# Optimization experiments

Hardware: AMD Instinct MI355X
Metric: run time of the kernel (lower is better)

The kernel has to match this reference:

```python
import jax, jax.numpy as jnp
import numpy as np

HEADS = 4
DIM_HEAD = 32


def setup_inputs() -> dict:
    key = jax.random.key(0)
    k1, k2, k3, k4, k5 = jax.random.split(key, 5)
    dim = 128
    hidden = HEADS * DIM_HEAD  # 128
    h = w = 384
    x = jax.random.normal(k1, (1, dim, h, w), dtype=jnp.float32)
    # 1x1 conv weights (eqx Conv2d layout: [out_c, in_c, 1, 1]) + biases
    w_qkv = jax.random.normal(k2, (3 * hidden, dim, 1, 1), dtype=jnp.float32) * (1.0 / np.sqrt(dim))
    b_qkv = jax.random.normal(k3, (3 * hidden,), dtype=jnp.float32) * 0.01
    w_out = jax.random.normal(k4, (dim, hidden, 1, 1), dtype=jnp.float32) * (1.0 / np.sqrt(hidden))
    b_out = jax.random.normal(k5, (dim,), dtype=jnp.float32) * 0.01
    return {"x": x, "w_qkv": w_qkv, "b_qkv": b_qkv, "w_out": w_out, "b_out": b_out}


def reference(x, w_qkv, b_qkv, w_out, b_out):
    b, c, h, w = x.shape  # b == 1 (module squeezes batch)
    xs = x[0]  # (c, h, w)
    # 1x1 conv == channel matmul
    qkv = jnp.einsum('oc,chw->ohw', w_qkv[:, :, 0, 0], xs) + b_qkv[:, None, None]
    # rearrange '(qkv heads c) h w -> qkv heads c (h w)'
    qkv = qkv.reshape(3, HEADS, DIM_HEAD, h * w)
    q, k, v = qkv[0], qkv[1], qkv[2]  # each (heads, d, n)
    k = jax.nn.softmax(k, axis=-1)
    # context: (heads, d, e) -- small per-head outer product accumulated over n
    context = jnp.einsum('hdn,hen->hde', k, v)
    out = jnp.einsum('hde,hdn->hen', context, q)  # (heads, e, n)
    out = out.reshape(HEADS * DIM_HEAD, h, w)
    y = jnp.einsum('oc,chw->ohw', w_out[:, :, 0, 0], out) + b_out[:, None, None]
    return y  # (dim, h, w) -- module returns squeezed output
```

## Files before the change

### kernel.cpp

```cpp
#include <hip/hip_runtime.h>
#include <hip/hip_bf16.h>
#include <stdint.h>


#define NPOS 147456
#define NTILES 2304
#define NB1 512

typedef __attribute__((ext_vector_type(8))) short short8;
typedef __attribute__((ext_vector_type(4))) float floatx4;

__device__ __forceinline__ uint16_t f2bf(float f) {
    uint32_t u = __float_as_uint(f);
    return (uint16_t)((u + 0x7fffu + ((u >> 16) & 1u)) >> 16);
}
__device__ __forceinline__ uint32_t pack2(float a, float b) {
#if __has_builtin(__builtin_amdgcn_cvt_pk_bf16_f32)
    auto r = __builtin_amdgcn_cvt_pk_bf16_f32(a, b);
    uint32_t u; __builtin_memcpy(&u, &r, sizeof(u));
    return u;
#else
    return (uint32_t)f2bf(a) | ((uint32_t)f2bf(b) << 16);
#endif
}

#define XS_STRIDE 68
#define PS_STRIDE 36
#define WST_STRIDE 132

__device__ __forceinline__ void k1_load(const float* __restrict__ xb, float* pf) {
    #pragma unroll
    for (int i = 0; i < 32; ++i) pf[i] = xb[(size_t)i * NPOS];
}
__device__ __forceinline__ void k1_store(uint32_t* Xsbuf, const float* pf, int lane, int c0) {
    #pragma unroll
    for (int i = 0; i < 8; ++i) {
        uint2 w;
        w.x = pack2(pf[i * 4 + 0], pf[i * 4 + 1]);
        w.y = pack2(pf[i * 4 + 2], pf[i * 4 + 3]);
        *(uint2*)&Xsbuf[lane * XS_STRIDE + (c0 + i * 4) / 2] = w;
    }
}
__device__ __forceinline__ void k1_tile(
    const uint32_t* __restrict__ Xsbuf, uint32_t* __restrict__ Psw,
    const short8 (&wfr)[4][4], const float (&biasv)[4],
    floatx4 (&acc2)[4], float (&sacc)[2], int m, int quad)
{
    #pragma unroll
    for (int nt = 0; nt < 4; ++nt) {
        short8 afr[4];
        #pragma unroll
        for (int ks = 0; ks < 4; ++ks)
            afr[ks] = *(const short8*)&Xsbuf[(nt * 16 + m) * XS_STRIDE + ks * 16 + quad * 4];
        floatx4 pa[4];
        #pragma unroll
        for (int kt = 0; kt < 4; ++kt) pa[kt] = (floatx4){0.f, 0.f, 0.f, 0.f};
        #pragma unroll
        for (int ks = 0; ks < 4; ++ks)
            #pragma unroll
            for (int kt = 0; kt < 4; ++kt)
                pa[kt] = __builtin_amdgcn_mfma_f32_16x16x32_bf16(afr[ks], wfr[kt][ks], pa[kt], 0, 0, 0);
        #pragma unroll
        for (int kt = 0; kt < 4; ++kt) {
            float v0 = pa[kt][0] + biasv[kt];
            float v1 = pa[kt][1] + biasv[kt];
            float v2 = pa[kt][2] + biasv[kt];
            float v3 = pa[kt][3] + biasv[kt];
            if (kt < 2) {
                v0 = __expf(v0); v1 = __expf(v1);
                v2 = __expf(v2); v3 = __expf(v3);
                sacc[kt] += (v0 + v1) + (v2 + v3);
            }
            uint2 w;
            w.x = pack2(v0, v1);
            w.y = pack2(v2, v3);
            *(uint2*)&Psw[(kt * 16 + m) * PS_STRIDE + nt * 8 + quad * 2] = w;
        }
    }
    #pragma unroll
    for (int ks = 0; ks < 2; ++ks) {
        short8 ea[2], vb[2];
        #pragma unroll
        for (int dt = 0; dt < 2; ++dt)
            ea[dt] = *(const short8*)&Psw[(dt * 16 + m) * PS_STRIDE + ks * 16 + quad * 4];
        #pragma unroll
        for (int et = 0; et < 2; ++et)
            vb[et] = *(const short8*)&Psw[(32 + et * 16 + m) * PS_STRIDE + ks * 16 + quad * 4];
        #pragma unroll
        for (int dt = 0; dt < 2; ++dt)
            #pragma unroll
            for (int et = 0; et < 2; ++et)
                acc2[dt * 2 + et] = __builtin_amdgcn_mfma_f32_16x16x32_bf16(ea[dt], vb[et], acc2[dt * 2 + et], 0, 0, 0);
    }
}

__global__ __launch_bounds__(256, 2) void k1_ctx(
    const float* __restrict__ x, const float* __restrict__ w_qkv,
    const float* __restrict__ b_qkv, float* __restrict__ ctxP, int nb1)
{
    __shared__ uint32_t smem[2 * 64 * XS_STRIDE + 256 * PS_STRIDE];
    uint32_t* const Xs0 = smem;
    uint32_t* const Xs1 = smem + 64 * XS_STRIDE;
    uint32_t* const Ps  = smem + 2 * 64 * XS_STRIDE;

    const int t = threadIdx.x;
    const int lane = t & 63;
    const int wavu = __builtin_amdgcn_readfirstlane(t >> 6);
    const int m = lane & 15, quad = lane >> 4;
    const int c0 = wavu * 32;
    uint32_t* const Psw = &Ps[wavu * 64 * PS_STRIDE];

    const int T0 = NTILES / nb1, R = NTILES % nb1;
    const int b = blockIdx.x;
    const int cnt_tiles = T0 + (b < R ? 1 : 0);
    const int s0 = (b < R) ? b * (T0 + 1) : R * (T0 + 1) + (b - R) * T0;

    const float* xw = x + (size_t)c0 * NPOS + lane;
    float pfA[32], pfB[32];

    k1_load(xw + (size_t)s0 * 64, pfA);

    short8 wfr[4][4];
    float biasv[4];
    float* const Wst = (float*)smem + wavu * (32 * WST_STRIDE);
    #pragma unroll
    for (int pass = 0; pass < 2; ++pass) {
        const int rbase = (pass == 0 ? 128 : 256) + wavu * 32;
        const float* g = w_qkv + (size_t)rbase * 128;
        #pragma unroll
        for (int i = 0; i < 64; ++i) {
            const int idx = i * 64 + lane;
            Wst[(idx >> 7) * WST_STRIDE + (idx & 127)] = g[idx];
        }
        __syncthreads();
        #pragma unroll
        for (int kt = 0; kt < 2; ++kt) {
            const int lr = kt * 16 + m;
            #pragma unroll
            for (int ks = 0; ks < 4; ++ks) {
                const float* p = &Wst[lr * WST_STRIDE + ks * 32 + quad * 8];
                float4 a = *(const float4*)p;
                float4 c = *(const float4*)(p + 4);
                short8 w;
                w[0] = (short)f2bf(a.x); w[1] = (short)f2bf(a.y);
                w[2] = (short)f2bf(a.z); w[3] = (short)f2bf(a.w);
                w[4] = (short)f2bf(c.x); w[5] = (short)f2bf(c.y);
                w[6] = (short)f2bf(c.z); w[7] = (short)f2bf(c.w);
                wfr[pass * 2 + kt][ks] = w;
            }
            biasv[pass * 2 + kt] = b_qkv[rbase + kt * 16 + m];
        }
        __syncthreads();
    }

    floatx4 acc2[4];
    #pragma unroll
    for (int i = 0; i < 4; ++i) acc2[i] = (floatx4){0.f, 0.f, 0.f, 0.f};
    float sacc[2] = {0.f, 0.f};

    if (cnt_tiles > 1) k1_load(xw + (size_t)(s0 + 1) * 64, pfB);
    k1_store(Xs0, pfA, lane, c0);
    __syncthreads();

    for (int i = 0; i < cnt_tiles; i += 2) {
        if (i + 2 < cnt_tiles) k1_load(xw + (size_t)(s0 + i + 2) * 64, pfA);
        k1_tile(Xs0, Psw, wfr, biasv, acc2, sacc, m, quad);
        if (i + 1 < cnt_tiles) k1_store(Xs1, pfB, lane, c0);
        __syncthreads();
        if (i + 1 < cnt_tiles) {
            if (i + 3 < cnt_tiles) k1_load(xw + (size_t)(s0 + i + 3) * 64, pfB);
            k1_tile(Xs1, Psw, wfr, biasv, acc2, sacc, m, quad);
            if (i + 2 < cnt_tiles) k1_store(Xs0, pfA, lane, c0);
            __syncthreads();
        }
    }

    float* __restrict__ dst = ctxP + (size_t)(b & 7) * 4224;
    #pragma unroll
    for (int dt = 0; dt < 2; ++dt)
        #pragma unroll
        for (int et = 0; et < 2; ++et)
            #pragma unroll
            for (int r = 0; r < 4; ++r) {
                const int d = dt * 16 + quad * 4 + r, e = et * 16 + m;
                atomicAdd(&dst[wavu * 1024 + d * 32 + e], acc2[dt * 2 + et][r]);
            }
    #pragma unroll
    for (int kt = 0; kt < 2; ++kt) {
        float s = sacc[kt];
        s += __shfl_down(s, 32, 64);
        s += __shfl_down(s, 16, 64);
        if (lane < 16) atomicAdd(&dst[4096 + wavu * 32 + kt * 16 + lane], s);
    }
}

__global__ __launch_bounds__(256) void k2bc(
    const float* __restrict__ ctxP, const float* __restrict__ w_out,
    const float* __restrict__ w_qkv, const float* __restrict__ b_qkv,
    const float* __restrict__ b_out, uint32_t* __restrict__ Bmb, float* __restrict__ cvec)
{
    __shared__ float ctx33[128 * 33];
    __shared__ float Ss[128];
    __shared__ float Arow[128];
    __shared__ float row[128];
    __shared__ float red[128];
    const int o = blockIdx.x, t = threadIdx.x;
    for (int j = t; j < 4224; j += 256) {
        float s = 0.f;
        #pragma unroll
        for (int p = 0; p < 8; ++p) s += ctxP[p * 4224 + j];
        if (j < 4096) ctx33[(j >> 5) * 33 + (j & 31)] = s;
        else          Ss[j - 4096] = s;
    }
    __syncthreads();
    if (t < 128) {
        const int h = t >> 5;
        float s = 0.f;
        #pragma unroll
        for (int e = 0; e < 32; ++e)
            s = fmaf(w_out[o * 128 + h * 32 + e], ctx33[t * 33 + e], s);
        Arow[t] = s / Ss[t];
    }
    __syncthreads();
    if (t < 128) {
        float s = 0.f;
        #pragma unroll 16
        for (int hd = 0; hd < 128; ++hd)
            s = fmaf(Arow[hd], w_qkv[hd * 128 + t], s);
        row[t] = s;
        red[t] = Arow[t] * b_qkv[t];
    }
    __syncthreads();
    if (t < 64) Bmb[o * 64 + t] = pack2(row[2 * t], row[2 * t + 1]);
    if (t == 0) {
        float cs = b_out[o];
        #pragma unroll 8
        for (int i = 0; i < 128; ++i) cs += red[i];
        cvec[o] = cs;
    }
}

__global__ __launch_bounds__(256) void k3(
    const float* __restrict__ x, const uint32_t* __restrict__ Bmb,
    const float* __restrict__ cvec, float* __restrict__ y)
{
    __shared__ uint32_t Xs[64 * XS_STRIDE];
    const int t = threadIdx.x, lane = t & 63;
    const int wavu = __builtin_amdgcn_readfirstlane(t >> 6);
    const int m = lane & 15, quad = lane >> 4;
    const int n0 = blockIdx.x * 64;
    const int c0 = wavu * 32;

    float pf[32];
    k1_load(x + (size_t)c0 * NPOS + n0 + lane, pf);

    short8 bfr[2][4];
    float cv[2];
    #pragma unroll
    for (int ot = 0; ot < 2; ++ot) {
        const int o = (wavu * 2 + ot) * 16 + m;
        cv[ot] = cvec[o];
        #pragma unroll
        for (int ks = 0; ks < 4; ++ks)
            bfr[ot][ks] = *(const short8*)&Bmb[o * 64 + ks * 16 + quad * 4];
    }
    k1_store(Xs, pf, lane, c0);
    __syncthreads();

    floatx4 acc[2][4];
    #pragma unroll
    for (int ot = 0; ot < 2; ++ot)
        #pragma unroll
        for (int nt = 0; nt < 4; ++nt) acc[ot][nt] = (floatx4){0.f, 0.f, 0.f, 0.f};
    #pragma unroll
    for (int nt = 0; nt < 4; ++nt) {
        short8 afr[4];
        #pragma unroll
        for (int ks = 0; ks < 4; ++ks)
            afr[ks] = *(const short8*)&Xs[(nt * 16 + m) * XS_STRIDE + ks * 16 + quad * 4];
        #pragma unroll
        for (int ks = 0; ks < 4; ++ks)
            #pragma unroll
            for (int ot = 0; ot < 2; ++ot)
                acc[ot][nt] = __builtin_amdgcn_mfma_f32_16x16x32_bf16(afr[ks], bfr[ot][ks], acc[ot][nt], 0, 0, 0);
    }
    #pragma unroll
    for (int ot = 0; ot < 2; ++ot) {
        const int o = (wavu * 2 + ot) * 16 + m;
        #pragma unroll
        for (int nt = 0; nt < 4; ++nt) {
            floatx4 v = acc[ot][nt];
            v.x += cv[ot]; v.y += cv[ot]; v.z += cv[ot]; v.w += cv[ot];
            *(floatx4*)(y + (size_t)o * NPOS + n0 + nt * 16 + quad * 4) = v;
        }
    }
}

extern "C" void kernel_launch(void* const* d_in, const int* in_sizes, int n_in,
                              void* d_out, int out_size, void* d_ws, size_t ws_size,
                              hipStream_t stream)
{
    const float* x     = (const float*)d_in[0];
    const float* w_qkv = (const float*)d_in[1];
    const float* b_qkv = (const float*)d_in[2];
    const float* w_out = (const float*)d_in[3];
    const float* b_out = (const float*)d_in[4];
    float* y = (float*)d_out;

    char* wsb = (char*)d_ws;
    float* ctxP    = (float*)wsb;
    uint32_t* Bmb  = (uint32_t*)(wsb + (size_t)8 * 4224 * 4);
    float* cvec    = (float*)(wsb + (size_t)8 * 4224 * 4 + (size_t)8192 * 4);

    hipMemsetAsync(ctxP, 0, (size_t)8 * 4224 * sizeof(float), stream);
    hipLaunchKernelGGL(k1_ctx, dim3(NB1), dim3(256), 0, stream, x, w_qkv, b_qkv, ctxP, NB1);
    hipLaunchKernelGGL(k2bc, dim3(128), dim3(256), 0, stream, ctxP, w_out, w_qkv, b_qkv, b_out, Bmb, cvec);
    hipLaunchKernelGGL(k3, dim3(NTILES), dim3(256), 0, stream, x, Bmb, cvec, y);
}
```

Measured before the change: 183.5 us.

## Fuse three kernels into one cooperative persistent kernel with grid syncs

Merges the context-reduction, weight-folding and output-projection kernels into one cooperative kernel that separates the phases with grid-wide barriers. Intermediate values are exchanged through relaxed agent-scope atomics. The output phase becomes persistent, with each block looping over several tiles and prefetching the next one. This is meant to remove kernel launch gaps and tail effects, at the cost of grid-sync overhead and idle blocks during the small middle phase. If the cooperative launch is not possible, it falls back to three separate kernels.

After: 261.9 us. +42.7%, slower.

```diff
diff --git a/kernel.cpp b/kernel.cpp
--- a/kernel.cpp
+++ b/kernel.cpp
@@ -1,7 +1,10 @@
 #include <hip/hip_runtime.h>
+#include <hip/hip_cooperative_groups.h>
 #include <hip/hip_bf16.h>
 #include <stdint.h>
 
+
+namespace cg = cooperative_groups;
 
 #define NPOS 147456
 #define NTILES 2304
@@ -22,6 +25,22 @@
 #else
     return (uint32_t)f2bf(a) | ((uint32_t)f2bf(b) << 16);
 #endif
+}
+
+__device__ __forceinline__ float aloadf(const float* p) {
+    return __hip_atomic_load(p, __ATOMIC_RELAXED, __HIP_MEMORY_SCOPE_AGENT);
+}
+__device__ __forceinline__ void astoref(float* p, float v) {
+    __hip_atomic_store(p, v, __ATOMIC_RELAXED, __HIP_MEMORY_SCOPE_AGENT);
+}
+__device__ __forceinline__ void astoreu(uint32_t* p, uint32_t v) {
+    __hip_atomic_store(p, v, __ATOMIC_RELAXED, __HIP_MEMORY_SCOPE_AGENT);
+}
+__device__ __forceinline__ short8 aload_s8(const uint32_t* p) {
+    union { uint64_t u[2]; short8 s; } c;
+    c.u[0] = __hip_atomic_load((const uint64_t*)p,       __ATOMIC_RELAXED, __HIP_MEMORY_SCOPE_AGENT);
+    c.u[1] = __hip_atomic_load((const uint64_t*)(p + 2), __ATOMIC_RELAXED, __HIP_MEMORY_SCOPE_AGENT);
+    return c.s;
 }
 
 #define XS_STRIDE 68
@@ -94,24 +113,17 @@
     }
 }
 
-__global__ __launch_bounds__(256, 2) void k1_ctx(
-    const float* __restrict__ x, const float* __restrict__ w_qkv,
-    const float* __restrict__ b_qkv, float* __restrict__ ctxP, int nb1)
-{
-    __shared__ uint32_t smem[2 * 64 * XS_STRIDE + 256 * PS_STRIDE];
+__device__ __forceinline__ void phase1(
+    uint32_t* smem, const float* __restrict__ x, const float* __restrict__ w_qkv,
+    const float* __restrict__ b_qkv, float* __restrict__ ctxP, int nb1,
+    int b, int t, int lane, int wavu, int m, int quad, int c0)
+{
     uint32_t* const Xs0 = smem;
     uint32_t* const Xs1 = smem + 64 * XS_STRIDE;
     uint32_t* const Ps  = smem + 2 * 64 * XS_STRIDE;
-
-    const int t = threadIdx.x;
-    const int lane = t & 63;
-    const int wavu = __builtin_amdgcn_readfirstlane(t >> 6);
-    const int m = lane & 15, quad = lane >> 4;
-    const int c0 = wavu * 32;
     uint32_t* const Psw = &Ps[wavu * 64 * PS_STRIDE];
 
     const int T0 = NTILES / nb1, R = NTILES % nb1;
-    const int b = blockIdx.x;
     const int cnt_tiles = T0 + (b < R ? 1 : 0);
     const int s0 = (b < R) ? b * (T0 + 1) : R * (T0 + 1) + (b - R) * T0;
 
@@ -194,21 +206,21 @@
     }
 }
 
-__global__ __launch_bounds__(256) void k2bc(
-    const float* __restrict__ ctxP, const float* __restrict__ w_out,
+__device__ __forceinline__ void phase3(
+    uint32_t* smem, const float* __restrict__ ctxP, const float* __restrict__ w_out,
     const float* __restrict__ w_qkv, const float* __restrict__ b_qkv,
-    const float* __restrict__ b_out, uint32_t* __restrict__ Bmb, float* __restrict__ cvec)
-{
-    __shared__ float ctx33[128 * 33];
-    __shared__ float Ss[128];
-    __shared__ float Arow[128];
-    __shared__ float row[128];
-    __shared__ float red[128];
-    const int o = blockIdx.x, t = threadIdx.x;
+    const float* __restrict__ b_out, uint32_t* __restrict__ Bmb,
+    float* __restrict__ cvec, int o, int t)
+{
+    float* const ctx33 = (float*)smem;
+    float* const Ss    = ctx33 + 128 * 33;
+    float* const Arow  = Ss + 128;
+    float* const rowS  = Arow + 128;
+    float* const red   = rowS + 128;
     for (int j = t; j < 4224; j += 256) {
         float s = 0.f;
         #pragma unroll
-        for (int p = 0; p < 8; ++p) s += ctxP[p * 4224 + j];
+        for (int p = 0; p < 8; ++p) s += aloadf(&ctxP[p * 4224 + j]);
         if (j < 4096) ctx33[(j >> 5) * 33 + (j & 31)] = s;
         else          Ss[j - 4096] = s;
     }
@@ -227,73 +239,133 @@
         #pragma unroll 16
         for (int hd = 0; hd < 128; ++hd)
             s = fmaf(Arow[hd], w_qkv[hd * 128 + t], s);
-        row[t] = s;
+        rowS[t] = s;
         red[t] = Arow[t] * b_qkv[t];
     }
     __syncthreads();
-    if (t < 64) Bmb[o * 64 + t] = pack2(row[2 * t], row[2 * t + 1]);
+    if (t < 64) astoreu(&Bmb[o * 64 + t], pack2(rowS[2 * t], rowS[2 * t + 1]));
     if (t == 0) {
         float cs = b_out[o];
         #pragma unroll 8
         for (int i = 0; i < 128; ++i) cs += red[i];
-        cvec[o] = cs;
-    }
-}
-
-__global__ __launch_bounds__(256) void k3(
-    const float* __restrict__ x, const uint32_t* __restrict__ Bmb,
-    const float* __restrict__ cvec, float* __restrict__ y)
-{
-    __shared__ uint32_t Xs[64 * XS_STRIDE];
+        astoref(&cvec[o], cs);
+    }
+}
+
+__device__ __forceinline__ void phase4(
+    uint32_t* smem, const float* __restrict__ x, const uint32_t* __restrict__ Bmb,
+    const float* __restrict__ cvec, float* __restrict__ y, int nb1,
+    int b, int lane, int wavu, int m, int quad, int c0)
+{
+    uint32_t* const Xs3 = smem;
+    const int T3 = NTILES / nb1, R3 = NTILES % nb1;
+    const int cnt3 = T3 + (b < R3 ? 1 : 0);
+    const int s03 = (b < R3) ? b * (T3 + 1) : R3 * (T3 + 1) + (b - R3) * T3;
+
+    short8 bfr[2][4];
+    float cv[2];
+    #pragma unroll
+    for (int ot = 0; ot < 2; ++ot) {
+        const int o = (wavu * 2 + ot) * 16 + m;
+        cv[ot] = aloadf(&cvec[o]);
+        #pragma unroll
+        for (int ks = 0; ks < 4; ++ks)
+            bfr[ot][ks] = aload_s8(&Bmb[o * 64 + ks * 16 + quad * 4]);
+    }
+
+    float pf[32];
+    k1_load(x + (size_t)c0 * NPOS + (size_t)s03 * 64 + lane, pf);
+
+    for (int s = 0; s < cnt3; ++s) {
+        if (s) __syncthreads();
+        k1_store(Xs3, pf, lane, c0);
+        __syncthreads();
+        if (s + 1 < cnt3)
+            k1_load(x + (size_t)c0 * NPOS + (size_t)(s03 + s + 1) * 64 + lane, pf);
+
+        const int n0 = (s03 + s) * 64;
+        floatx4 acc[2][4];
+        #pragma unroll
+        for (int ot = 0; ot < 2; ++ot)
+            #pragma unroll
+            for (int nt = 0; nt < 4; ++nt) acc[ot][nt] = (floatx4){0.f, 0.f, 0.f, 0.f};
+        #pragma unroll
+        for (int nt = 0; nt < 4; ++nt) {
+            short8 afr[4];
+            #pragma unroll
+            for (int ks = 0; ks < 4; ++ks)
+                afr[ks] = *(const short8*)&Xs3[(nt * 16 + m) * XS_STRIDE + ks * 16 + quad * 4];
+            #pragma unroll
+            for (int ks = 0; ks < 4; ++ks)
+                #pragma unroll
+                for (int ot = 0; ot < 2; ++ot)
+                    acc[ot][nt] = __builtin_amdgcn_mfma_f32_16x16x32_bf16(afr[ks], bfr[ot][ks], acc[ot][nt], 0, 0, 0);
+        }
+        #pragma unroll
+        for (int ot = 0; ot < 2; ++ot) {
+            const int o = (wavu * 2 + ot) * 16 + m;
+            #pragma unroll
+            for (int nt = 0; nt < 4; ++nt) {
+                floatx4 v = acc[ot][nt];
+                v.x += cv[ot]; v.y += cv[ot]; v.z += cv[ot]; v.w += cv[ot];
+                *(floatx4*)(y + (size_t)o * NPOS + n0 + nt * 16 + quad * 4) = v;
+            }
+        }
+    }
+}
+
+__global__ __launch_bounds__(256, 2) void mono(
+    const float* __restrict__ x, const float* __restrict__ w_qkv,
+    const float* __restrict__ b_qkv, const float* __restrict__ w_out,
+    const float* __restrict__ b_out, float* __restrict__ ctxP,
+    uint32_t* __restrict__ Bmb, float* __restrict__ cvec,
+    float* __restrict__ y, int nb1)
+{
+    __shared__ uint32_t smem[2 * 64 * XS_STRIDE + 256 * PS_STRIDE];
+    const int t = threadIdx.x;
+    const int lane = t & 63;
+    const int wavu = __builtin_amdgcn_readfirstlane(t >> 6);
+    const int m = lane & 15, quad = lane >> 4;
+    const int c0 = wavu * 32;
+    const int b = blockIdx.x;
+
+    phase1(smem, x, w_qkv, b_qkv, ctxP, nb1, b, t, lane, wavu, m, quad, c0);
+    cg::this_grid().sync();
+    if (b < 128) phase3(smem, ctxP, w_out, w_qkv, b_qkv, b_out, Bmb, cvec, b, t);
+    cg::this_grid().sync();
+    phase4(smem, x, Bmb, cvec, y, nb1, b, lane, wavu, m, quad, c0);
+}
+
+__global__ __launch_bounds__(256, 2) void k1s(
+    const float* __restrict__ x, const float* __restrict__ w_qkv,
+    const float* __restrict__ b_qkv, float* __restrict__ ctxP, int nb1)
+{
+    __shared__ uint32_t smem[2 * 64 * XS_STRIDE + 256 * PS_STRIDE];
     const int t = threadIdx.x, lane = t & 63;
     const int wavu = __builtin_amdgcn_readfirstlane(t >> 6);
-    const int m = lane & 15, quad = lane >> 4;
-    const int n0 = blockIdx.x * 64;
-    const int c0 = wavu * 32;
-
-    float pf[32];
-    k1_load(x + (size_t)c0 * NPOS + n0 + lane, pf);
-
-    short8 bfr[2][4];
-    float cv[2];
-    #pragma unroll
-    for (int ot = 0; ot < 2; ++ot) {
-        const int o = (wavu * 2 + ot) * 16 + m;
-        cv[ot] = cvec[o];
-        #pragma unroll
-        for (int ks = 0; ks < 4; ++ks)
-            bfr[ot][ks] = *(const short8*)&Bmb[o * 64 + ks * 16 + quad * 4];
-    }
-    k1_store(Xs, pf, lane, c0);
-    __syncthreads();
-
-    floatx4 acc[2][4];
-    #pragma unroll
-    for (int ot = 0; ot < 2; ++ot)
-        #pragma unroll
-        for (int nt = 0; nt < 4; ++nt) acc[ot][nt] = (floatx4){0.f, 0.f, 0.f, 0.f};
-    #pragma unroll
-    for (int nt = 0; nt < 4; ++nt) {
-        short8 afr[4];
-        #pragma unroll
-        for (int ks = 0; ks < 4; ++ks)
-            afr[ks] = *(const short8*)&Xs[(nt * 16 + m) * XS_STRIDE + ks * 16 + quad * 4];
-        #pragma unroll
-        for (int ks = 0; ks < 4; ++ks)
-            #pragma unroll
-            for (int ot = 0; ot < 2; ++ot)
-                acc[ot][nt] = __builtin_amdgcn_mfma_f32_16x16x32_bf16(afr[ks], bfr[ot][ks], acc[ot][nt], 0, 0, 0);
-    }
-    #pragma unroll
-    for (int ot = 0; ot < 2; ++ot) {
-        const int o = (wavu * 2 + ot) * 16 + m;
-        #pragma unroll
-        for (int nt = 0; nt < 4; ++nt) {
-            floatx4 v = acc[ot][nt];
-            v.x += cv[ot]; v.y += cv[ot]; v.z += cv[ot]; v.w += cv[ot];
-            *(floatx4*)(y + (size_t)o * NPOS + n0 + nt * 16 + quad * 4) = v;
-        }
-    }
+    phase1(smem, x, w_qkv, b_qkv, ctxP, nb1, blockIdx.x, t, lane, wavu,
+           lane & 15, lane >> 4, wavu * 32);
+}
+
+__global__ __launch_bounds__(256) void k2s(
+    const float* __restrict__ ctxP, const float* __restrict__ w_out,
+    const float* __restrict__ w_qkv, const float* __restrict__ b_qkv,
+    const float* __restrict__ b_out, uint32_t* __restrict__ Bmb,
+    float* __restrict__ cvec)
+{
+    __shared__ uint32_t smem[4736];
+    phase3(smem, ctxP, w_out, w_qkv, b_qkv, b_out, Bmb, cvec, blockIdx.x, threadIdx.x);
+}
+
+__global__ __launch_bounds__(256) void k3s(
+    const float* __restrict__ x, const uint32_t* __restrict__ Bmb,
+    const float* __restrict__ cvec, float* __restrict__ y, int nb1)
+{
+    __shared__ uint32_t smem[64 * XS_STRIDE];
+    const int t = threadIdx.x, lane = t & 63;
+    const int wavu = __builtin_amdgcn_readfirstlane(t >> 6);
+    phase4(smem, x, Bmb, cvec, y, nb1, blockIdx.x, lane, wavu,
+           lane & 15, lane >> 4, wavu * 32);
 }
 
 extern "C" void kernel_launch(void* const* d_in, const int* in_sizes, int n_in,
@@ -313,7 +385,27 @@
     float* cvec    = (float*)(wsb + (size_t)8 * 4224 * 4 + (size_t)8192 * 4);
 
     hipMemsetAsync(ctxP, 0, (size_t)8 * 4224 * sizeof(float), stream);
-    hipLaunchKernelGGL(k1_ctx, dim3(NB1), dim3(256), 0, stream, x, w_qkv, b_qkv, ctxP, NB1);
-    hipLaunchKernelGGL(k2bc, dim3(128), dim3(256), 0, stream, ctxP, w_out, w_qkv, b_qkv, b_out, Bmb, cvec);
-    hipLaunchKernelGGL(k3, dim3(NTILES), dim3(256), 0, stream, x, Bmb, cvec, y);
-}
+
+    static int coopBlocks = -1;
+    if (coopBlocks < 0) {
+        int nb = 0;
+        hipError_t e = hipOccupancyMaxActiveBlocksPerMultiprocessor(&nb, mono, 256, 0);
+        coopBlocks = (e == hipSuccess) ? nb * 256 : 0;
+    }
+
+    int grid = coopBlocks > NB1 ? NB1 : coopBlocks;
+    if (grid >= 256) {
+        int nb1c = grid;
+        void* args[] = { (void*)&x, (void*)&w_qkv, (void*)&b_qkv, (void*)&w_out,
+                         (void*)&b_out, (void*)&ctxP, (void*)&Bmb, (void*)&cvec,
+                         (void*)&y, (void*)&nb1c };
+        hipError_t e = hipLaunchCooperativeKernel((void*)mono, dim3(grid), dim3(256),
+                                                  args, 0, stream);
+        if (e == hipSuccess) return;
+        (void)hipGetLastError();
+    }
+
+    hipLaunchKernelGGL(k1s, dim3(NB1), dim3(256), 0, stream, x, w_qkv, b_qkv, ctxP, NB1);
+    hipLaunchKernelGGL(k2s, dim3(128), dim3(256), 0, stream, ctxP, w_out, w_qkv, b_qkv, b_out, Bmb, cvec);
+    hipLaunchKernelGGL(k3s, dim3(NB1), dim3(256), 0, stream, x, Bmb, cvec, y, NB1);
+}
```

## Fuse context reduction and output-matrix build into k1 via last-block counter

Applied to the files above, without the earlier changes.

Removes the separate k2bc launch by having the last k1 block, detected via an atomic completion counter, sum the partial contexts and compute the folded output weight matrix and bias vector. This saves one kernel launch and its gap. In exchange, that tail work runs serially on a single 256-thread block, processing output rows in four chunks of 32, where k2bc previously spread it over 128 blocks.

After: 310.7 us. +69.3%, slower.

```diff
diff --git a/kernel.cpp b/kernel.cpp
--- a/kernel.cpp
+++ b/kernel.cpp
@@ -22,6 +22,9 @@
 #else
     return (uint32_t)f2bf(a) | ((uint32_t)f2bf(b) << 16);
 #endif
+}
+__device__ __forceinline__ float aloadf(const float* p) {
+    return __hip_atomic_load(p, __ATOMIC_RELAXED, __HIP_MEMORY_SCOPE_AGENT);
 }
 
 #define XS_STRIDE 68
@@ -94,149 +97,172 @@
     }
 }
 
-__global__ __launch_bounds__(256, 2) void k1_ctx(
+__global__ __launch_bounds__(256, 2) void k1f(
     const float* __restrict__ x, const float* __restrict__ w_qkv,
-    const float* __restrict__ b_qkv, float* __restrict__ ctxP, int nb1)
+    const float* __restrict__ b_qkv, const float* __restrict__ w_out,
+    const float* __restrict__ b_out, float* __restrict__ ctxP,
+    int* __restrict__ cnt, uint32_t* __restrict__ Bmb,
+    float* __restrict__ cvec, int nb1)
 {
     __shared__ uint32_t smem[2 * 64 * XS_STRIDE + 256 * PS_STRIDE];
-    uint32_t* const Xs0 = smem;
-    uint32_t* const Xs1 = smem + 64 * XS_STRIDE;
-    uint32_t* const Ps  = smem + 2 * 64 * XS_STRIDE;
+    __shared__ int lastFlag;
 
     const int t = threadIdx.x;
     const int lane = t & 63;
     const int wavu = __builtin_amdgcn_readfirstlane(t >> 6);
     const int m = lane & 15, quad = lane >> 4;
     const int c0 = wavu * 32;
-    uint32_t* const Psw = &Ps[wavu * 64 * PS_STRIDE];
-
-    const int T0 = NTILES / nb1, R = NTILES % nb1;
     const int b = blockIdx.x;
-    const int cnt_tiles = T0 + (b < R ? 1 : 0);
-    const int s0 = (b < R) ? b * (T0 + 1) : R * (T0 + 1) + (b - R) * T0;
-
-    const float* xw = x + (size_t)c0 * NPOS + lane;
-    float pfA[32], pfB[32];
-
-    k1_load(xw + (size_t)s0 * 64, pfA);
-
-    short8 wfr[4][4];
-    float biasv[4];
-    float* const Wst = (float*)smem + wavu * (32 * WST_STRIDE);
-    #pragma unroll
-    for (int pass = 0; pass < 2; ++pass) {
-        const int rbase = (pass == 0 ? 128 : 256) + wavu * 32;
-        const float* g = w_qkv + (size_t)rbase * 128;
-        #pragma unroll
-        for (int i = 0; i < 64; ++i) {
-            const int idx = i * 64 + lane;
-            Wst[(idx >> 7) * WST_STRIDE + (idx & 127)] = g[idx];
-        }
+
+    {
+        uint32_t* const Xs0 = smem;
+        uint32_t* const Xs1 = smem + 64 * XS_STRIDE;
+        uint32_t* const Ps  = smem + 2 * 64 * XS_STRIDE;
+        uint32_t* const Psw = &Ps[wavu * 64 * PS_STRIDE];
+
+        const int T0 = NTILES / nb1, R = NTILES % nb1;
+        const int cnt_tiles = T0 + (b < R ? 1 : 0);
+        const int s0 = (b < R) ? b * (T0 + 1) : R * (T0 + 1) + (b - R) * T0;
+
+        const float* xw = x + (size_t)c0 * NPOS + lane;
+        float pfA[32], pfB[32];
+
+        k1_load(xw + (size_t)s0 * 64, pfA);
+
+        short8 wfr[4][4];
+        float biasv[4];
+        float* const Wst = (float*)smem + wavu * (32 * WST_STRIDE);
+        #pragma unroll
+        for (int pass = 0; pass < 2; ++pass) {
+            const int rbase = (pass == 0 ? 128 : 256) + wavu * 32;
+            const float* g = w_qkv + (size_t)rbase * 128;
+            #pragma unroll
+            for (int i = 0; i < 64; ++i) {
+                const int idx = i * 64 + lane;
+                Wst[(idx >> 7) * WST_STRIDE + (idx & 127)] = g[idx];
+            }
+            __syncthreads();
+            #pragma unroll
+            for (int kt = 0; kt < 2; ++kt) {
+                const int lr = kt * 16 + m;
+                #pragma unroll
+                for (int ks = 0; ks < 4; ++ks) {
+                    const float* p = &Wst[lr * WST_STRIDE + ks * 32 + quad * 8];
+                    float4 a = *(const float4*)p;
+                    float4 c = *(const float4*)(p + 4);
+                    short8 w;
+                    w[0] = (short)f2bf(a.x); w[1] = (short)f2bf(a.y);
+                    w[2] = (short)f2bf(a.z); w[3] = (short)f2bf(a.w);
+                    w[4] = (short)f2bf(c.x); w[5] = (short)f2bf(c.y);
+                    w[6] = (short)f2bf(c.z); w[7] = (short)f2bf(c.w);
+                    wfr[pass * 2 + kt][ks] = w;
+                }
+                biasv[pass * 2 + kt] = b_qkv[rbase + kt * 16 + m];
+            }
+            __syncthreads();
+        }
+
+        floatx4 acc2[4];
+        #pragma unroll
+        for (int i = 0; i < 4; ++i) acc2[i] = (floatx4){0.f, 0.f, 0.f, 0.f};
+        float sacc[2] = {0.f, 0.f};
+
+        if (cnt_tiles > 1) k1_load(xw + (size_t)(s0 + 1) * 64, pfB);
+        k1_store(Xs0, pfA, lane, c0);
         __syncthreads();
+
+        for (int i = 0; i < cnt_tiles; i += 2) {
+            if (i + 2 < cnt_tiles) k1_load(xw + (size_t)(s0 + i + 2) * 64, pfA);
+            k1_tile(Xs0, Psw, wfr, biasv, acc2, sacc, m, quad);
+            if (i + 1 < cnt_tiles) k1_store(Xs1, pfB, lane, c0);
+            __syncthreads();
+            if (i + 1 < cnt_tiles) {
+                if (i + 3 < cnt_tiles) k1_load(xw + (size_t)(s0 + i + 3) * 64, pfB);
+                k1_tile(Xs1, Psw, wfr, biasv, acc2, sacc, m, quad);
+                if (i + 2 < cnt_tiles) k1_store(Xs0, pfA, lane, c0);
+                __syncthreads();
+            }
+        }
+
+        float* __restrict__ dst = ctxP + (size_t)(b & 7) * 4224;
+        #pragma unroll
+        for (int dt = 0; dt < 2; ++dt)
+            #pragma unroll
+            for (int et = 0; et < 2; ++et)
+                #pragma unroll
+                for (int r = 0; r < 4; ++r) {
+                    const int d = dt * 16 + quad * 4 + r, e = et * 16 + m;
+                    atomicAdd(&dst[wavu * 1024 + d * 32 + e], acc2[dt * 2 + et][r]);
+                }
         #pragma unroll
         for (int kt = 0; kt < 2; ++kt) {
-            const int lr = kt * 16 + m;
-            #pragma unroll
-            for (int ks = 0; ks < 4; ++ks) {
-                const float* p = &Wst[lr * WST_STRIDE + ks * 32 + quad * 8];
-                float4 a = *(const float4*)p;
-                float4 c = *(const float4*)(p + 4);
-                short8 w;
-                w[0] = (short)f2bf(a.x); w[1] = (short)f2bf(a.y);
-                w[2] = (short)f2bf(a.z); w[3] = (short)f2bf(a.w);
-                w[4] = (short)f2bf(c.x); w[5] = (short)f2bf(c.y);
-                w[6] = (short)f2bf(c.z); w[7] = (short)f2bf(c.w);
-                wfr[pass * 2 + kt][ks] = w;
-            }
-            biasv[pass * 2 + kt] = b_qkv[rbase + kt * 16 + m];
-        }
-        __syncthreads();
-    }
-
-    floatx4 acc2[4];
-    #pragma unroll
-    for (int i = 0; i < 4; ++i) acc2[i] = (floatx4){0.f, 0.f, 0.f, 0.f};
-    float sacc[2] = {0.f, 0.f};
-
-    if (cnt_tiles > 1) k1_load(xw + (size_t)(s0 + 1) * 64, pfB);
-    k1_store(Xs0, pfA, lane, c0);
-    __syncthreads();
-
-    for (int i = 0; i < cnt_tiles; i += 2) {
-        if (i + 2 < cnt_tiles) k1_load(xw + (size_t)(s0 + i + 2) * 64, pfA);
-        k1_tile(Xs0, Psw, wfr, biasv, acc2, sacc, m, quad);
-        if (i + 1 < cnt_tiles) k1_store(Xs1, pfB, lane, c0);
-        __syncthreads();
-        if (i + 1 < cnt_tiles) {
-            if (i + 3 < cnt_tiles) k1_load(xw + (size_t)(s0 + i + 3) * 64, pfB);
-            k1_tile(Xs1, Psw, wfr, biasv, acc2, sacc, m, quad);
-            if (i + 2 < cnt_tiles) k1_store(Xs0, pfA, lane, c0);
-            __syncthreads();
-        }
-    }
-
-    float* __restrict__ dst = ctxP + (size_t)(b & 7) * 4224;
-    #pragma unroll
-    for (int dt = 0; dt < 2; ++dt)
-        #pragma unroll
-        for (int et = 0; et < 2; ++et)
-            #pragma unroll
-            for (int r = 0; r < 4; ++r) {
-                const int d = dt * 16 + quad * 4 + r, e = et * 16 + m;
-                atomicAdd(&dst[wavu * 1024 + d * 32 + e], acc2[dt * 2 + et][r]);
-            }
-    #pragma unroll
-    for (int kt = 0; kt < 2; ++kt) {
-        float s = sacc[kt];
-        s += __shfl_down(s, 32, 64);
-        s += __shfl_down(s, 16, 64);
-        if (lane < 16) atomicAdd(&dst[4096 + wavu * 32 + kt * 16 + lane], s);
-    }
-}
-
-__global__ __launch_bounds__(256) void k2bc(
-    const float* __restrict__ ctxP, const float* __restrict__ w_out,
-    const float* __restrict__ w_qkv, const float* __restrict__ b_qkv,
-    const float* __restrict__ b_out, uint32_t* __restrict__ Bmb, float* __restrict__ cvec)
-{
-    __shared__ float ctx33[128 * 33];
-    __shared__ float Ss[128];
-    __shared__ float Arow[128];
-    __shared__ float row[128];
-    __shared__ float red[128];
-    const int o = blockIdx.x, t = threadIdx.x;
+            float s = sacc[kt];
+            s += __shfl_down(s, 32, 64);
+            s += __shfl_down(s, 16, 64);
+            if (lane < 16) atomicAdd(&dst[4096 + wavu * 32 + kt * 16 + lane], s);
+        }
+    }
+
+    asm volatile("s_waitcnt vmcnt(0)" ::: "memory");
+    __syncthreads();
+    if (t == 0) {
+        const int old = atomicAdd(cnt, 1);
+        lastFlag = (old == nb1 - 1);
+    }
+    __syncthreads();
+    if (!lastFlag) return;
+
+    float* const ctx33 = (float*)smem;
+    float* const Ssl   = ctx33 + 4224;
+    float* const invS  = Ssl + 128;
+    float* const A32   = invS + 128;
     for (int j = t; j < 4224; j += 256) {
         float s = 0.f;
         #pragma unroll
-        for (int p = 0; p < 8; ++p) s += ctxP[p * 4224 + j];
+        for (int p = 0; p < 8; ++p) s += aloadf(&ctxP[p * 4224 + j]);
         if (j < 4096) ctx33[(j >> 5) * 33 + (j & 31)] = s;
-        else          Ss[j - 4096] = s;
-    }
-    __syncthreads();
-    if (t < 128) {
-        const int h = t >> 5;
-        float s = 0.f;
-        #pragma unroll
-        for (int e = 0; e < 32; ++e)
-            s = fmaf(w_out[o * 128 + h * 32 + e], ctx33[t * 33 + e], s);
-        Arow[t] = s / Ss[t];
-    }
-    __syncthreads();
-    if (t < 128) {
-        float s = 0.f;
-        #pragma unroll 16
-        for (int hd = 0; hd < 128; ++hd)
-            s = fmaf(Arow[hd], w_qkv[hd * 128 + t], s);
-        row[t] = s;
-        red[t] = Arow[t] * b_qkv[t];
-    }
-    __syncthreads();
-    if (t < 64) Bmb[o * 64 + t] = pack2(row[2 * t], row[2 * t + 1]);
-    if (t == 0) {
-        float cs = b_out[o];
-        #pragma unroll 8
-        for (int i = 0; i < 128; ++i) cs += red[i];
-        cvec[o] = cs;
+        else          Ssl[j - 4096] = s;
+    }
+    __syncthreads();
+    if (t < 128) invS[t] = 1.0f / Ssl[t];
+    __syncthreads();
+
+    const int hd = t & 127, oh = t >> 7;
+    for (int oc = 0; oc < 4; ++oc) {
+        const int ob = oc * 32;
+        {
+            const int h = hd >> 5;
+            for (int oi = oh; oi < 32; oi += 2) {
+                const int o = ob + oi;
+                float s = 0.f;
+                #pragma unroll
+                for (int e = 0; e < 32; ++e)
+                    s = fmaf(w_out[o * 128 + h * 32 + e], ctx33[hd * 33 + e], s);
+                A32[oi * 129 + hd] = s * invS[hd];
+            }
+        }
+        __syncthreads();
+        {
+            const int c = hd;
+            for (int oi = oh; oi < 32; oi += 2) {
+                const int o = ob + oi;
+                float s = 0.f;
+                #pragma unroll 16
+                for (int k = 0; k < 128; ++k)
+                    s = fmaf(A32[oi * 129 + k], w_qkv[k * 128 + c], s);
+                const float shi = __shfl_down(s, 1, 64);
+                if ((t & 1) == 0) Bmb[o * 64 + (c >> 1)] = pack2(s, shi);
+            }
+        }
+        if (t < 32) {
+            const int o = ob + t;
+            float cs = b_out[o];
+            #pragma unroll 16
+            for (int k = 0; k < 128; ++k)
+                cs = fmaf(A32[t * 129 + k], b_qkv[k], cs);
+            cvec[o] = cs;
+        }
+        __syncthreads();
     }
 }
 
@@ -308,12 +334,13 @@
     float* y = (float*)d_out;
 
     char* wsb = (char*)d_ws;
-    float* ctxP    = (float*)wsb;
-    uint32_t* Bmb  = (uint32_t*)(wsb + (size_t)8 * 4224 * 4);
-    float* cvec    = (float*)(wsb + (size_t)8 * 4224 * 4 + (size_t)8192 * 4);
-
-    hipMemsetAsync(ctxP, 0, (size_t)8 * 4224 * sizeof(float), stream);
-    hipLaunchKernelGGL(k1_ctx, dim3(NB1), dim3(256), 0, stream, x, w_qkv, b_qkv, ctxP, NB1);
-    hipLaunchKernelGGL(k2bc, dim3(128), dim3(256), 0, stream, ctxP, w_out, w_qkv, b_qkv, b_out, Bmb, cvec);
+    float* ctxP   = (float*)wsb;
+    int* cnt      = (int*)(ctxP + 8 * 4224);
+    uint32_t* Bmb = (uint32_t*)(cnt + 4);
+    float* cvec   = (float*)(Bmb + 8192);
+
+    hipMemsetAsync(ctxP, 0, (size_t)8 * 4224 * 4 + 16, stream);
+    hipLaunchKernelGGL(k1f, dim3(NB1), dim3(256), 0, stream,
+                       x, w_qkv, b_qkv, w_out, b_out, ctxP, cnt, Bmb, cvec, NB1);
     hipLaunchKernelGGL(k3, dim3(NTILES), dim3(256), 0, stream, x, Bmb, cvec, y);
 }
```
